# Optimization experiments

Measured on AMD Instinct MI355X. Metric: run time of the kernel, lower is better.

## Reference

```python
import jax, jax.numpy as jnp
import numpy as np

NUM_TOKENS = 8192
TOKEN_DIM = 256
N = 65536
TOPK = 5
DECAY = 0.1      # cur_decay (set_decay_updates never called -> stays at init decay)
EPS = 1e-5
TEMP = 1.0


def setup_inputs() -> dict:
    key = jax.random.key(0)
    k1, k2 = jax.random.split(key)
    return {
        "inputs_flatten": jax.random.normal(k1, (N, TOKEN_DIM), dtype=jnp.float32),
        "embed": jax.random.normal(k2, (NUM_TOKENS, TOKEN_DIM), dtype=jnp.float32),
        "cluster_size": jnp.zeros((NUM_TOKENS,), dtype=jnp.float32),
        "cluster_sum": jnp.zeros((NUM_TOKENS,), dtype=jnp.float32),
        "embed_avg": jnp.zeros((NUM_TOKENS, TOKEN_DIM), dtype=jnp.float32),
    }


def reference(inputs_flatten, embed, cluster_size, cluster_sum, embed_avg):
    x = inputs_flatten                              # [N, D]
    # squared euclidean distances to codebook: [N, K]
    distances = (jnp.sum(x * x, axis=1, keepdims=True)
                 + jnp.sum(embed * embed, axis=1)
                 - 2.0 * (x @ embed.T))
    # top-k nearest codes (smallest distance)
    neg_topk, topk_idx = jax.lax.top_k(-distances, TOPK)   # [N, k]
    topk_dist = -neg_topk
    weights = jax.nn.softmax(-topk_dist / TEMP, axis=1)    # [N, k]
    # scatter soft weights into dense one-hot-ish encodings [N, K]
    rows = jnp.arange(x.shape[0])[:, None]
    encodings = jnp.zeros_like(distances).at[rows, topk_idx].set(weights)
    encoding_indices = jnp.argmax(encodings, axis=1)[:, None]   # [N, 1]

    # training-mode EMA codebook update (module default is training=True)
    encoding_sum = jnp.sum(encodings, axis=0)                   # [K]
    new_cluster_sum = cluster_sum + encoding_sum
    new_cluster_size = cluster_size * DECAY + encoding_sum * (1.0 - DECAY)
    embed_sum = encodings.T @ x                                 # [K, D]
    new_embed_avg = embed_avg * DECAY + embed_sum * (1.0 - DECAY)
    smoothed = (new_cluster_size + EPS) / (jnp.sum(new_cluster_size) + NUM_TOKENS * EPS)
    cs = smoothed * jnp.sum(new_cluster_size)
    new_embed = new_embed_avg / cs[:, None]                     # embed.data.copy_(...)

    quantize = encodings @ new_embed                            # [N, D]
    quantize = jax.lax.stop_gradient(quantize - x) + x          # straight-through
    return quantize, encoding_indices
```

## Files before the change

kernel.cpp:

```cpp
#include <hip/hip_runtime.h>
#include <hip/hip_bf16.h>
#include <math.h>
#include <limits.h>

#define NROWS 65536
#define DIM   256
#define NCODE 8192
#define NTOPK 5

typedef __attribute__((ext_vector_type(4))) float     f32x4;
typedef __attribute__((ext_vector_type(4))) int       i32x4;
typedef __attribute__((ext_vector_type(2))) unsigned  u32x2;

#define WS_ESWZ   0u
#define WS_CINIT  2097152u
#define WS_CAND   2129920u
#define WS_IDX5   4227072u
#define WS_W5     5537792u
#define WS_ENCSUM 6848512u
#define WS_CNT    6881280u
#define WS_OFFS   6914048u
#define WS_CURS   6946816u
#define WS_SFAC   6979584u
#define WS_ENTR   6979840u
#define WS_NEWEMB 9601280u

#define ENT_PER_BLK 64
#define NENT (NROWS * NTOPK)

__device__ __forceinline__ void gl_lds16(const void* g, void* l) {
  __builtin_amdgcn_global_load_lds(
      (const __attribute__((address_space(1))) unsigned int*)g,
      (__attribute__((address_space(3))) unsigned int*)l, 16, 0, 0);
}

__device__ __forceinline__ unsigned f2key(float f) {
  unsigned u = __float_as_uint(f);
  return (u & 0x80000000u) ? ~u : (u | 0x80000000u);
}
__device__ __forceinline__ float key2f(unsigned k) {
  unsigned u = (k & 0x80000000u) ? (k ^ 0x80000000u) : ~k;
  return __uint_as_float(u);
}

__global__ __launch_bounds__(256) void k_prep(const float* __restrict__ embed,
                                              signed char* __restrict__ eswz,
                                              int* __restrict__ cinit) {
  const int code = blockIdx.x;
  const int d = threadIdx.x;
  float v = embed[code * DIM + d];
  float qf = fminf(127.f, fmaxf(-127.f, rintf(16.f * v)));
  int q = (int)qf;
  __shared__ unsigned char rb[256];
  __shared__ int red[4];
  rb[d] = (unsigned char)(q & 255);
  int e2 = q * q;
  #pragma unroll
  for (int off = 32; off; off >>= 1) e2 += __shfl_down(e2, off);
  const int lane = d & 63, w = d >> 6;
  if (lane == 0) red[w] = e2;
  __syncthreads();
  if (d == 0) cinit[code] = -((red[0] + red[1] + red[2] + red[3]) >> 1);
  if (d < 64) {
    unsigned u = (unsigned)rb[4 * d] | ((unsigned)rb[4 * d + 1] << 8) |
                 ((unsigned)rb[4 * d + 2] << 16) | ((unsigned)rb[4 * d + 3] << 24);
    const int cs = (d >> 2) ^ (code & 15);
    ((unsigned*)(eswz + code * 256))[(cs << 2) | (d & 3)] = u;
  }
}


struct PList { int a, b, c, d; };

__device__ __forceinline__ void ladder(PList& P, int t) {
  int c0 = min(P.a, t); P.a = max(P.a, t);
  int c1 = min(P.b, c0); P.b = max(P.b, c0);
  int c2 = min(P.c, c1); P.c = max(P.c, c1);
  P.d = max(P.d, c2);
}

__device__ __forceinline__ void psel(PList& P, i32x4 acc, i32x4 en, int cb) {
  int p0 = ((acc[0] + en[0]) << 13) + cb;
  int p1 = ((acc[1] + en[1]) << 13) + cb + 1;
  int p2 = ((acc[2] + en[2]) << 13) + cb + 2;
  int p3 = ((acc[3] + en[3]) << 13) + cb + 3;
  int h1 = max(p0, p1), l1 = min(p0, p1);
  int h2 = max(p2, p3), l2 = min(p2, p3);
  int t1 = max(h1, h2);
  int t2 = max(min(h1, h2), max(l1, l2));
  ladder(P, t1);
  if (__any(t2 > P.d)) ladder(P, t2);
}

__device__ __forceinline__ int pk4(f32x4 v) {
  int r = 0;
  #pragma unroll
  for (int j = 0; j < 4; ++j) {
    float q = fminf(127.f, fmaxf(-127.f, rintf(16.f * v[j])));
    r |= ((int)q & 255) << (8 * j);
  }
  return r;
}

__global__ __launch_bounds__(256, 4) void k_gemm(const float* __restrict__ x,
                                                 const signed char* __restrict__ eswz,
                                                 const int* __restrict__ cinit,
                                                 unsigned short* __restrict__ cand) {
  __shared__ signed char ebuf[3][8192];
  const int tid = threadIdx.x;
  const int lane = tid & 63, wave = tid >> 6;
  const int q = lane >> 4, ln = lane & 15;
  const int row = blockIdx.x * 64 + wave * 16 + ln;

  gl_lds16(eswz + tid * 16, &ebuf[0][tid * 16]);
  gl_lds16(eswz + 4096 + tid * 16, &ebuf[0][4096 + tid * 16]);

  i32x4 enc0 = *(const i32x4*)(cinit + q * 4);
  i32x4 enc1 = *(const i32x4*)(cinit + 16 + q * 4);

  i32x4 xf[4];
  {
    const float* xr = x + (unsigned)row * DIM;
    #pragma unroll
    for (int s = 0; s < 4; ++s) {
      i32x4 dw;
      #pragma unroll
      for (int d = 0; d < 4; ++d)
        dw[d] = pk4(*(const f32x4*)(xr + s * 64 + q * 16 + d * 4));
      xf[s] = dw;
    }
  }

  PList P0 = {INT_MIN, INT_MIN, INT_MIN, INT_MIN};
  PList P1 = P0;

  int slot = 0;
  #pragma unroll 1
  for (int it = 0; it < 256; ++it) {
    const int nslot = (slot + 1 == 3) ? 0 : slot + 1;
    const int tl = (it < 255) ? it + 1 : 255;
    const signed char* src = eswz + (unsigned)tl * 8192;
    gl_lds16(src + tid * 16, &ebuf[nslot][tid * 16]);
    gl_lds16(src + 4096 + tid * 16, &ebuf[nslot][4096 + tid * 16]);
    i32x4 enn0 = *(const i32x4*)(cinit + tl * 32 + q * 4);
    i32x4 enn1 = *(const i32x4*)(cinit + tl * 32 + 16 + q * 4);

    asm volatile("s_waitcnt vmcnt(4)\n\ts_barrier" ::: "memory");

    const signed char* eb = ebuf[slot];
    i32x4 acc0 = {0, 0, 0, 0}, acc1 = {0, 0, 0, 0};
    #pragma unroll
    for (int s = 0; s < 4; ++s) {
      const int chunk = (4 * s + q) ^ ln;
      i32x4 ea0 = *(const i32x4*)&eb[ln * 256 + chunk * 16];
      i32x4 ea1 = *(const i32x4*)&eb[4096 + ln * 256 + chunk * 16];
      acc0 = __builtin_amdgcn_mfma_i32_16x16x64_i8(ea0, xf[s], acc0, 0, 0, 0);
      acc1 = __builtin_amdgcn_mfma_i32_16x16x64_i8(ea1, xf[s], acc1, 0, 0, 0);
    }
    psel(P0, acc0, enc0, it * 32 + q * 4);
    psel(P1, acc1, enc1, it * 32 + 16 + q * 4);

    enc0 = enn0; enc1 = enn1;
    slot = nslot;
  }

  ladder(P0, P1.a); ladder(P0, P1.b); ladder(P0, P1.c); ladder(P0, P1.d);

  u32x2 pk;
  pk[0] = ((unsigned)P0.a & 8191u) | (((unsigned)P0.b & 8191u) << 16);
  pk[1] = ((unsigned)P0.c & 8191u) | (((unsigned)P0.d & 8191u) << 16);
  *(u32x2*)&cand[row * 16 + q * 4] = pk;
}

__global__ __launch_bounds__(256) void k_refine(const float* __restrict__ x,
                                                const float* __restrict__ embed,
                                                const unsigned short* __restrict__ cand,
                                                float* __restrict__ out_idx,
                                                int* __restrict__ idx5,
                                                float* __restrict__ w5,
                                                float* __restrict__ enc_sum,
                                                unsigned* __restrict__ cnt) {
  __shared__ float sh[4][16][66];
  const int wave = threadIdx.x >> 6, l = threadIdx.x & 63;
  const int row = blockIdx.x * 4 + wave;
  const float* xr = x + (unsigned)row * DIM;
  const f32x4 xv = *(const f32x4*)(xr + 4 * l);
  const float t0 = -2.f * xv[0], t1 = -2.f * xv[1];
  const float t2 = -2.f * xv[2], t3 = -2.f * xv[3];

  int cd[16];
  const unsigned* cp = (const unsigned*)(cand + row * 16);
  #pragma unroll
  for (int i = 0; i < 8; ++i) {
    unsigned v = cp[i];
    cd[2 * i] = (int)(v & 0xFFFFu);
    cd[2 * i + 1] = (int)(v >> 16);
  }

  #pragma unroll
  for (int ci = 0; ci < 16; ++ci) {
    const f32x4 e = *(const f32x4*)(embed + (unsigned)cd[ci] * DIM + 4 * l);
    float p = e[0] * (e[0] + t0);
    p = fmaf(e[1], e[1] + t1, p);
    p = fmaf(e[2], e[2] + t2, p);
    p = fmaf(e[3], e[3] + t3, p);
    sh[wave][ci][l] = p;
  }
  asm volatile("s_waitcnt lgkmcnt(0)" ::: "memory");

  const int c = l >> 2, sub = l & 3;
  const float* sp = &sh[wave][c][sub * 16];
  double s64 = 0.0;
  #pragma unroll
  for (int i = 0; i < 4; ++i) {
    f32x4 v = *(const f32x4*)(sp + i * 4);
    s64 += (double)v[0] + (double)v[1] + (double)v[2] + (double)v[3];
  }
  s64 += __shfl_xor(s64, 1);
  s64 += __shfl_xor(s64, 2);

  double sc = __shfl(s64, (l & 15) * 4);
  unsigned key = f2key((float)sc);
  const int myc = cd[l & 15];

  bool used = false;
  int codes[5]; float svals[5];
  #pragma unroll
  for (int j = 0; j < 5; ++j) {
    unsigned k = used ? 0xFFFFFFFFu : key;
    unsigned mm = k;
    #pragma unroll
    for (int off = 1; off < 16; off <<= 1) mm = min(mm, (unsigned)__shfl_xor((int)mm, off));
    int cc = (k == mm) ? myc : 0x7FFFFFFF;
    #pragma unroll
    for (int off = 1; off < 16; off <<= 1) cc = min(cc, __shfl_xor(cc, off));
    used = used || (myc == cc);
    codes[j] = cc;
    svals[j] = key2f(mm);
  }

  float ex[5], sum = 0.f;
  #pragma unroll
  for (int j = 0; j < 5; ++j) { ex[j] = expf(-(svals[j] - svals[0])); sum += ex[j]; }
  const float inv = 1.f / sum;

  if (l == 0) {
    out_idx[row] = (float)codes[0];
    #pragma unroll
    for (int j = 0; j < 5; ++j) {
      float w = ex[j] * inv;
      idx5[row * 5 + j] = codes[j];
      w5[row * 5 + j] = w;
      atomicAdd(&enc_sum[codes[j]], w);
      atomicAdd(&cnt[codes[j]], 1u);
    }
  }
}

__global__ __launch_bounds__(256) void k_scan(const unsigned* __restrict__ cnt,
                                              unsigned* __restrict__ offs,
                                              unsigned* __restrict__ cursor,
                                              const float* __restrict__ enc_sum,
                                              const float* __restrict__ cluster_size,
                                              float* __restrict__ sfac) {
  __shared__ unsigned part[256];
  __shared__ double sred[256];
  const int t = threadIdx.x;
  unsigned s = 0;
  for (int i = 0; i < 32; ++i) s += cnt[t * 32 + i];
  part[t] = s;
  double ds = 0.0;
  for (int i = t; i < NCODE; i += 256)
    ds += 0.1 * (double)cluster_size[i] + 0.9 * (double)enc_sum[i];
  sred[t] = ds;
  __syncthreads();
  if (t == 0) {
    unsigned run = 0;
    for (int i = 0; i < 256; ++i) { unsigned tmp = part[i]; part[i] = run; run += tmp; }
    double S = 0.0;
    for (int i = 0; i < 256; ++i) S += sred[i];
    sfac[0] = (float)(S / (S + (double)NCODE * 1e-5));
  }
  __syncthreads();
  unsigned off = part[t];
  for (int i = 0; i < 32; ++i) {
    unsigned c = cnt[t * 32 + i];
    offs[t * 32 + i] = off;
    cursor[t * 32 + i] = off;
    off += c;
  }
}

__global__ __launch_bounds__(256) void k_fill(const int* __restrict__ idx5,
                                              const float* __restrict__ w5,
                                              unsigned* __restrict__ cursor,
                                              uint2* __restrict__ entries) {
  const int i = blockIdx.x * 256 + threadIdx.x;
  if (i >= NENT) return;
  const unsigned c = (unsigned)idx5[i];
  const float w = w5[i];
  const unsigned row = (unsigned)i / 5u;
  const unsigned slot = atomicAdd(&cursor[c], 1u);
  entries[slot] = make_uint2((c << 16) | row, __float_as_uint(w));
}

__global__ __launch_bounds__(256) void k_accum2(const float* __restrict__ x,
                                                const uint2* __restrict__ entries,
                                                float* __restrict__ embsum) {
  __shared__ uint2 ent[ENT_PER_BLK];
  const int t = threadIdx.x;
  const unsigned base = blockIdx.x * ENT_PER_BLK;
  if (t < ENT_PER_BLK * 2)
    ((unsigned*)ent)[t] = ((const unsigned*)(entries + base))[t];
  __syncthreads();

  float acc = 0.f;
  unsigned cur = ent[0].x >> 16;
  #pragma unroll 8
  for (int i = 0; i < ENT_PER_BLK; ++i) {
    const uint2 e = ent[i];
    const unsigned code = e.x >> 16;
    const unsigned row = e.x & 0xFFFFu;
    const float w = __uint_as_float(e.y);
    if (code != cur) {
      atomicAdd(&embsum[cur * DIM + t], acc);
      acc = 0.f; cur = code;
    }
    acc = fmaf(w, x[row * DIM + t], acc);
  }
  atomicAdd(&embsum[cur * DIM + t], acc);
}

__global__ __launch_bounds__(256) void k_norm(const float* __restrict__ embed_avg,
                                              const float* __restrict__ cluster_size,
                                              const float* __restrict__ enc_sum,
                                              const float* __restrict__ sfac,
                                              float* __restrict__ embsum ) {
  const int k = blockIdx.x, d = threadIdx.x;
  const float ncs = 0.1f * cluster_size[k] + 0.9f * enc_sum[k];
  const float cs = (ncs + 1e-5f) * sfac[0];
  const unsigned o = (unsigned)k * DIM + d;
  embsum[o] = (0.1f * embed_avg[o] + 0.9f * embsum[o]) / cs;
}

__global__ __launch_bounds__(256) void k_quant(const int* __restrict__ idx5,
                                               const float* __restrict__ w5,
                                               const float* __restrict__ newemb,
                                               float* __restrict__ out) {
  const int d = threadIdx.x;
  const int rb = blockIdx.x * 16;
  #pragma unroll 2
  for (int r = 0; r < 16; ++r) {
    const int row = rb + r;
    float acc = 0.f;
    #pragma unroll
    for (int j = 0; j < 5; ++j)
      acc = fmaf(w5[row * 5 + j], newemb[(unsigned)idx5[row * 5 + j] * DIM + d], acc);
    out[(unsigned)row * DIM + d] = acc;
  }
}

extern "C" void kernel_launch(void* const* d_in, const int* in_sizes, int n_in,
                              void* d_out, int out_size, void* d_ws, size_t ws_size,
                              hipStream_t stream) {
  const float* x            = (const float*)d_in[0];
  const float* embed        = (const float*)d_in[1];
  const float* cluster_size = (const float*)d_in[2];
  const float* embed_avg    = (const float*)d_in[4];

  char* w = (char*)d_ws;
  signed char*    eswz   = (signed char*)(w + WS_ESWZ);
  int*            cinit  = (int*)(w + WS_CINIT);
  unsigned short* cand   = (unsigned short*)(w + WS_CAND);
  int*            idx5   = (int*)(w + WS_IDX5);
  float*          w5     = (float*)(w + WS_W5);
  float*          encsum = (float*)(w + WS_ENCSUM);
  unsigned*       cnt    = (unsigned*)(w + WS_CNT);
  unsigned*       offs   = (unsigned*)(w + WS_OFFS);
  unsigned*       curs   = (unsigned*)(w + WS_CURS);
  float*          sfac   = (float*)(w + WS_SFAC);
  uint2*          entr   = (uint2*)(w + WS_ENTR);
  float*          embsum = (float*)(w + WS_NEWEMB);

  float* out_q   = (float*)d_out;
  float* out_idx = out_q + (size_t)NROWS * DIM;

  hipMemsetAsync(w + WS_ENCSUM, 0, 65536, stream);
  hipMemsetAsync(w + WS_NEWEMB, 0, (size_t)NCODE * DIM * 4, stream);

  k_prep<<<NCODE, 256, 0, stream>>>(embed, eswz, cinit);
  k_gemm<<<NROWS / 64, 256, 0, stream>>>(x, eswz, cinit, cand);
  k_refine<<<NROWS / 4, 256, 0, stream>>>(x, embed, cand, out_idx, idx5, w5, encsum, cnt);
  k_scan<<<1, 256, 0, stream>>>(cnt, offs, curs, encsum, cluster_size, sfac);
  k_fill<<<(NENT + 255) / 256, 256, 0, stream>>>(idx5, w5, curs, entr);
  k_accum2<<<NENT / ENT_PER_BLK, 256, 0, stream>>>(x, entr, embsum);
  k_norm<<<NCODE, 256, 0, stream>>>(embed_avg, cluster_size, encsum, sfac, embsum);
  k_quant<<<NROWS / 16, 256, 0, stream>>>(idx5, w5, embsum, out_q);
}
```

Measured before the change: 489.3 us.

## Process two 16-row tiles per wave in int8 GEMM top-k and add early-exit selection

```diff
diff --git a/kernel.cpp b/kernel.cpp
--- a/kernel.cpp
+++ b/kernel.cpp
@@ -84,12 +84,15 @@
   int p1 = ((acc[1] + en[1]) << 13) + cb + 1;
   int p2 = ((acc[2] + en[2]) << 13) + cb + 2;
   int p3 = ((acc[3] + en[3]) << 13) + cb + 3;
-  int h1 = max(p0, p1), l1 = min(p0, p1);
-  int h2 = max(p2, p3), l2 = min(p2, p3);
+  int h1 = max(p0, p1);
+  int h2 = max(p2, p3);
   int t1 = max(h1, h2);
-  int t2 = max(min(h1, h2), max(l1, l2));
-  ladder(P, t1);
-  if (__any(t2 > P.d)) ladder(P, t2);
+  if (__any(t1 > P.d)) {
+    int l1 = min(p0, p1), l2 = min(p2, p3);
+    int t2 = max(min(h1, h2), max(l1, l2));
+    ladder(P, t1);
+    if (__any(t2 > P.d)) ladder(P, t2);
+  }
 }
 
 __device__ __forceinline__ int pk4(f32x4 v) {
@@ -102,7 +105,7 @@
   return r;
 }
 
-__global__ __launch_bounds__(256, 4) void k_gemm(const float* __restrict__ x,
+__global__ __launch_bounds__(256, 2) void k_gemm(const float* __restrict__ x,
                                                  const signed char* __restrict__ eswz,
                                                  const int* __restrict__ cinit,
                                                  unsigned short* __restrict__ cand) {
@@ -110,7 +113,7 @@
   const int tid = threadIdx.x;
   const int lane = tid & 63, wave = tid >> 6;
   const int q = lane >> 4, ln = lane & 15;
-  const int row = blockIdx.x * 64 + wave * 16 + ln;
+  const int wrow0 = blockIdx.x * 128 + wave * 32;
 
   gl_lds16(eswz + tid * 16, &ebuf[0][tid * 16]);
   gl_lds16(eswz + 4096 + tid * 16, &ebuf[0][4096 + tid * 16]);
@@ -118,16 +121,17 @@
   i32x4 enc0 = *(const i32x4*)(cinit + q * 4);
   i32x4 enc1 = *(const i32x4*)(cinit + 16 + q * 4);
 
-  i32x4 xf[4];
-  {
-    const float* xr = x + (unsigned)row * DIM;
+  i32x4 xf[2][4];
+  #pragma unroll
+  for (int t = 0; t < 2; ++t) {
+    const float* xr = x + (unsigned)(wrow0 + t * 16 + ln) * DIM;
     #pragma unroll
     for (int s = 0; s < 4; ++s) {
       i32x4 dw;
       #pragma unroll
       for (int d = 0; d < 4; ++d)
         dw[d] = pk4(*(const f32x4*)(xr + s * 64 + q * 16 + d * 4));
-      xf[s] = dw;
+      xf[t][s] = dw;
     }
   }
 
@@ -148,28 +152,38 @@
     asm volatile("s_waitcnt vmcnt(4)\n\ts_barrier" ::: "memory");
 
     const signed char* eb = ebuf[slot];
-    i32x4 acc0 = {0, 0, 0, 0}, acc1 = {0, 0, 0, 0};
+    i32x4 a00 = {0, 0, 0, 0}, a01 = a00, a10 = a00, a11 = a00;
     #pragma unroll
     for (int s = 0; s < 4; ++s) {
       const int chunk = (4 * s + q) ^ ln;
       i32x4 ea0 = *(const i32x4*)&eb[ln * 256 + chunk * 16];
       i32x4 ea1 = *(const i32x4*)&eb[4096 + ln * 256 + chunk * 16];
-      acc0 = __builtin_amdgcn_mfma_i32_16x16x64_i8(ea0, xf[s], acc0, 0, 0, 0);
-      acc1 = __builtin_amdgcn_mfma_i32_16x16x64_i8(ea1, xf[s], acc1, 0, 0, 0);
+      a00 = __builtin_amdgcn_mfma_i32_16x16x64_i8(ea0, xf[0][s], a00, 0, 0, 0);
+      a10 = __builtin_amdgcn_mfma_i32_16x16x64_i8(ea0, xf[1][s], a10, 0, 0, 0);
+      a01 = __builtin_amdgcn_mfma_i32_16x16x64_i8(ea1, xf[0][s], a01, 0, 0, 0);
+      a11 = __builtin_amdgcn_mfma_i32_16x16x64_i8(ea1, xf[1][s], a11, 0, 0, 0);
     }
-    psel(P0, acc0, enc0, it * 32 + q * 4);
-    psel(P1, acc1, enc1, it * 32 + 16 + q * 4);
+    const int cb0 = it * 32 + q * 4, cb1 = cb0 + 16;
+    psel(P0, a00, enc0, cb0);
+    psel(P0, a01, enc1, cb1);
+    psel(P1, a10, enc0, cb0);
+    psel(P1, a11, enc1, cb1);
 
     enc0 = enn0; enc1 = enn1;
     slot = nslot;
   }
 
-  ladder(P0, P1.a); ladder(P0, P1.b); ladder(P0, P1.c); ladder(P0, P1.d);
-
-  u32x2 pk;
-  pk[0] = ((unsigned)P0.a & 8191u) | (((unsigned)P0.b & 8191u) << 16);
-  pk[1] = ((unsigned)P0.c & 8191u) | (((unsigned)P0.d & 8191u) << 16);
-  *(u32x2*)&cand[row * 16 + q * 4] = pk;
+  {
+    const int row0 = wrow0 + ln;
+    u32x2 pk;
+    pk[0] = ((unsigned)P0.a & 8191u) | (((unsigned)P0.b & 8191u) << 16);
+    pk[1] = ((unsigned)P0.c & 8191u) | (((unsigned)P0.d & 8191u) << 16);
+    *(u32x2*)&cand[row0 * 16 + q * 4] = pk;
+    const int row1 = wrow0 + 16 + ln;
+    pk[0] = ((unsigned)P1.a & 8191u) | (((unsigned)P1.b & 8191u) << 16);
+    pk[1] = ((unsigned)P1.c & 8191u) | (((unsigned)P1.d & 8191u) << 16);
+    *(u32x2*)&cand[row1 * 16 + q * 4] = pk;
+  }
 }
 
 __global__ __launch_bounds__(256) void k_refine(const float* __restrict__ x,
@@ -389,7 +403,7 @@
   hipMemsetAsync(w + WS_NEWEMB, 0, (size_t)NCODE * DIM * 4, stream);
 
   k_prep<<<NCODE, 256, 0, stream>>>(embed, eswz, cinit);
-  k_gemm<<<NROWS / 64, 256, 0, stream>>>(x, eswz, cinit, cand);
+  k_gemm<<<NROWS / 128, 256, 0, stream>>>(x, eswz, cinit, cand);
   k_refine<<<NROWS / 4, 256, 0, stream>>>(x, embed, cand, out_idx, idx5, w5, encsum, cnt);
   k_scan<<<1, 256, 0, stream>>>(cnt, offs, curs, encsum, cluster_size, sfac);
   k_fill<<<(NENT + 255) / 256, 256, 0, stream>>>(idx5, w5, curs, entr);
```

After: 466.3 us. 1.05x faster.
